# Optimization experiments

Hardware: AMD Instinct MI355X
Metric: run time of the kernel (lower is better)

Reference implementation:

```python
import jax, jax.numpy as jnp
import numpy as np

WINDOW_SIZE = 7
C1 = 0.01 ** 2
C2 = 0.03 ** 2


def _gaussian_window(ws: int) -> jnp.ndarray:
    sigma = ws / 6.0
    coords = jnp.arange(ws, dtype=jnp.float32) - ws // 2
    g = jnp.exp(-coords ** 2 / (2 * sigma ** 2))
    g = g / g.sum()
    k3 = g[:, None, None] * g[None, :, None] * g[None, None, :]
    k3 = k3 / k3.sum()
    return k3.reshape(1, 1, ws, ws, ws)  # OIDHW


def _conv3d_same(x, w):
    pad = WINDOW_SIZE // 2
    return jax.lax.conv_general_dilated(
        x, w, window_strides=(1, 1, 1),
        padding=[(pad, pad)] * 3,
        dimension_numbers=('NCDHW', 'OIDHW', 'NCDHW'))


def setup_inputs() -> dict:
    key = jax.random.key(0)
    k1, k2 = jax.random.split(key)
    shape = (2, 1, 160, 160, 160)
    predicted = jax.random.uniform(k1, shape, dtype=jnp.float32)
    target = jax.random.uniform(k2, shape, dtype=jnp.float32)
    return {"predicted": predicted, "target": target}


def reference(predicted, target):
    window = _gaussian_window(WINDOW_SIZE)
    mu1 = _conv3d_same(predicted, window)
    mu2 = _conv3d_same(target, window)
    mu1_sq = mu1 ** 2
    mu2_sq = mu2 ** 2
    mu1_mu2 = mu1 * mu2
    sigma1_sq = _conv3d_same(predicted ** 2, window) - mu1_sq
    sigma2_sq = _conv3d_same(target ** 2, window) - mu2_sq
    sigma12 = _conv3d_same(predicted * target, window) - mu1_mu2
    ssim_map = ((2 * mu1_mu2 + C1) * (2 * sigma12 + C2)) / (
        (mu1_sq + mu2_sq + C1) * (sigma1_sq + sigma2_sq + C2))
    return 1.0 - ssim_map.mean()
```

## Files before the change

kernel.cpp:

```cpp
#include <hip/hip_runtime.h>
#include <math.h>

#define DD 160
#define HH 160
#define WW 160
#define NB 2
#define NEL (NB*DD*HH*WW)

#define XT 32
#define YT 16
#define ZC 10
#define NTHR 256
#define NZCH (DD/ZC)
#define GX (WW/XT)
#define GY (HH/YT)
#define NBLK (GX*GY*NB*NZCH)
#define NPART NBLK

#define HR 22
#define NJOB (HR*8)
#define CP 35

typedef float v2f __attribute__((ext_vector_type(2)));

struct G7 { float g[7]; };

__global__ __launch_bounds__(NTHR, 4) void ssim_fused(
        const float* __restrict__ p, const float* __restrict__ t,
        float* __restrict__ partial, G7 gw) {
    const int tid = threadIdx.x;
    const int tx  = tid & 31;
    const int tyo = tid >> 5;

    const int flat = blockIdx.x;
    const int w = (flat & 7) * (NBLK / 8) + (flat >> 3);
    const int bx = w % GX;
    const int by = (w / GX) % GY;
    const int bz = w / (GX * GY);

    const int x0 = bx * XT;
    const int y0 = by * YT;
    const int n  = bz / NZCH;
    const int zs = (bz % NZCH) * ZC;

    __shared__ float4 c4[2][HR][CP];

    v2f r01[2][6], r23[2][6];
#pragma unroll
    for (int yo = 0; yo < 2; ++yo)
#pragma unroll
        for (int j = 0; j < 6; ++j) {
            r01[yo][j] = (v2f)(0.f);
            r23[yo][j] = (v2f)(0.f);
        }

    const float C1v = 1e-4f, C2v = 9e-4f;
    float ssum = 0.f;
    const int hw = HH * WW;
    const float* pv = p + (size_t)n * DD * hw;
    const float* tv = t + (size_t)n * DD * hw;

    const int br = tid >> 3;
    const int bxg = tid & 7;
    const int bgy = y0 + br - 3;
    const bool browok = (unsigned)bgy < (unsigned)HH && tid < NJOB;
    const int cbase = x0 + 4 * bxg - 4;
    const int pcr = tx + (tx >> 3);
    bool qok[3];
#pragma unroll
    for (int q = 0; q < 3; ++q)
        qok[q] = browok && (unsigned)(cbase + 4 * q) < (unsigned)WW;

    const float* prow = pv + (size_t)(zs - 3) * hw + bgy * WW;
    const float* trow = tv + (size_t)(zs - 3) * hw + bgy * WW;

    float4 pfa[3], pfb[3];
    auto prefetch = [&](int sx) {
#pragma unroll
        for (int q = 0; q < 3; ++q) {
            pfa[q] = make_float4(0.f, 0.f, 0.f, 0.f);
            pfb[q] = make_float4(0.f, 0.f, 0.f, 0.f);
        }
        if (sx >= 0 && sx < DD && sx < zs + ZC + 3) {
#pragma unroll
            for (int q = 0; q < 3; ++q) {
                if (qok[q]) {
                    pfa[q] = *(const float4*)(prow + cbase + 4 * q);
                    pfb[q] = *(const float4*)(trow + cbase + 4 * q);
                }
            }
        }
    };

    prefetch(zs - 3);

    for (int s = zs - 3; s < zs + ZC + 3; ++s) {
        const int par = s & 1;
        const bool valid = (s >= 0) && (s < DD);

        if (valid) {
            if (tid < NJOB) {
                v2f s01[4], s23[4];
#pragma unroll
                for (int e = 0; e < 4; ++e) { s01[e] = (v2f)(0.f); s23[e] = (v2f)(0.f); }
#pragma unroll
                for (int q = 0; q < 3; ++q) {
                    const float af[4] = {pfa[q].x, pfa[q].y, pfa[q].z, pfa[q].w};
                    const float bf[4] = {pfb[q].x, pfb[q].y, pfb[q].z, pfb[q].w};
#pragma unroll
                    for (int j = 0; j < 4; ++j) {
                        const int i = 4 * q + j;
                        v2f pt; pt[0] = af[j]; pt[1] = bf[j];
                        v2f ud; ud[0] = af[j] + bf[j]; ud[1] = af[j] - bf[j];
                        v2f qu = ud * ud;
#pragma unroll
                        for (int e = 0; e < 4; ++e) {
                            const int k = i - e - 1;
                            if (k >= 0 && k < 7) {
                                s01[e] = gw.g[k] * pt + s01[e];
                                s23[e] = gw.g[k] * qu + s23[e];
                            }
                        }
                    }
                }
#pragma unroll
                for (int e = 0; e < 4; ++e) {
                    int c = 4 * bxg + e;
                    c4[par][br][c + (c >> 3)] =
                        make_float4(s01[e][0], s01[e][1], s23[e][0], s23[e][1]);
                }
            }
            __syncthreads();
        }

        prow += hw; trow += hw;
        prefetch(s + 1);

        v2f m01[2], m23[2];
#pragma unroll
        for (int yo = 0; yo < 2; ++yo) {
            m01[yo] = (v2f)(0.f);
            m23[yo] = (v2f)(0.f);
        }

        if (valid) {
#pragma unroll
            for (int r8 = 0; r8 < 8; ++r8) {
                float4 v = c4[par][2 * tyo + r8][pcr];
                v2f v01; v01[0] = v.x; v01[1] = v.y;
                v2f v23; v23[0] = v.z; v23[1] = v.w;
                if (r8 < 7) {
                    float w2 = gw.g[r8];
                    m01[0] = w2 * v01 + m01[0];
                    m23[0] = w2 * v23 + m23[0];
                }
                if (r8 > 0) {
                    float w2 = gw.g[r8 - 1];
                    m01[1] = w2 * v01 + m01[1];
                    m23[1] = w2 * v23 + m23[1];
                }
            }
        }

#pragma unroll
        for (int yo = 0; yo < 2; ++yo) {
            v2f v01 = m01[yo], v23 = m23[yo];
            v2f cons01 = gw.g[6] * v01 + r01[yo][0];
            v2f cons23 = gw.g[6] * v23 + r23[yo][0];
#pragma unroll
            for (int j = 0; j < 5; ++j) {
                r01[yo][j] = gw.g[5 - j] * v01 + r01[yo][j + 1];
                r23[yo][j] = gw.g[5 - j] * v23 + r23[yo][j + 1];
            }
            r01[yo][5] = gw.g[0] * v01;
            r23[yo][5] = gw.g[0] * v23;

            if (s >= zs + 3) {
                float mu1 = cons01[0], mu2 = cons01[1];
                float Eu  = cons23[0], Ew  = cons23[1];
                float mu12 = mu1 * mu2, mu1sq = mu1 * mu1, mu2sq = mu2 * mu2;
                float sumsq = 0.5f  * (Eu + Ew) - mu1sq - mu2sq;
                float s12   = 0.25f * (Eu - Ew) - mu12;
                float num = (2.f * mu12 + C1v) * (2.f * s12 + C2v);
                float den = (mu1sq + mu2sq + C1v) * (sumsq + C2v);
                ssum += num * __builtin_amdgcn_rcpf(den);
            }
        }
    }

#pragma unroll
    for (int off = 32; off > 0; off >>= 1)
        ssum += __shfl_down(ssum, off, 64);
    __shared__ float wsum[4];
    if ((tid & 63) == 0) wsum[tid >> 6] = ssum;
    __syncthreads();
    if (tid == 0)
        partial[flat] = wsum[0] + wsum[1] + wsum[2] + wsum[3];
}

__global__ __launch_bounds__(256) void ssim_final(
        const float* __restrict__ partial, float* __restrict__ out) {
    float s = 0.f;
    for (int i = threadIdx.x; i < NPART; i += 256) s += partial[i];
#pragma unroll
    for (int off = 32; off > 0; off >>= 1)
        s += __shfl_down(s, off, 64);
    __shared__ float wsum[4];
    int lane = threadIdx.x & 63, wid = threadIdx.x >> 6;
    if (lane == 0) wsum[wid] = s;
    __syncthreads();
    if (threadIdx.x == 0) {
        float tot = wsum[0] + wsum[1] + wsum[2] + wsum[3];
        out[0] = 1.0f - tot / (float)NEL;
    }
}

extern "C" void kernel_launch(void* const* d_in, const int* in_sizes, int n_in,
                              void* d_out, int out_size, void* d_ws, size_t ws_size,
                              hipStream_t stream) {
    const float* p = (const float*)d_in[0];
    const float* t = (const float*)d_in[1];
    float* out = (float*)d_out;
    float* partial = (float*)d_ws;

    G7 gw;
    {
        double s = 0.0, sig = 7.0 / 6.0;
        double g[7];
        for (int i = 0; i < 7; ++i) {
            double d = (double)i - 3.0;
            g[i] = exp(-d * d / (2.0 * sig * sig));
            s += g[i];
        }
        for (int i = 0; i < 7; ++i) gw.g[i] = (float)(g[i] / s);
    }

    ssim_fused<<<NBLK, NTHR, 0, stream>>>(p, t, partial, gw);
    ssim_final<<<1, 256, 0, stream>>>(partial, out);
}
```

Baseline: 144.1 us.

## Software-pipeline the horizontal pass, balance jobs across waves, lengthen z chunks

```diff
diff --git a/kernel.cpp b/kernel.cpp
--- a/kernel.cpp
+++ b/kernel.cpp
@@ -9,7 +9,7 @@
 
 #define XT 32
 #define YT 16
-#define ZC 10
+#define ZC 16
 #define NTHR 256
 #define NZCH (DD/ZC)
 #define GX (WW/XT)
@@ -19,6 +19,7 @@
 
 #define HR 22
 #define NJOB (HR*8)
+#define NJOBW 44
 #define CP 35
 
 typedef float v2f __attribute__((ext_vector_type(2)));
@@ -42,6 +43,7 @@
     const int y0 = by * YT;
     const int n  = bz / NZCH;
     const int zs = (bz % NZCH) * ZC;
+    const int send = zs + ZC + 3;
 
     __shared__ float4 c4[2][HR][CP];
 
@@ -60,10 +62,13 @@
     const float* pv = p + (size_t)n * DD * hw;
     const float* tv = t + (size_t)n * DD * hw;
 
-    const int br = tid >> 3;
-    const int bxg = tid & 7;
+    const int lane = tid & 63, wv = tid >> 6;
+    const int j = wv * NJOBW + lane;
+    const bool jok = lane < NJOBW;
+    const int br  = j >> 3;
+    const int bxg = j & 7;
     const int bgy = y0 + br - 3;
-    const bool browok = (unsigned)bgy < (unsigned)HH && tid < NJOB;
+    const bool browok = jok && (unsigned)bgy < (unsigned)HH;
     const int cbase = x0 + 4 * bxg - 4;
     const int pcr = tx + (tx >> 3);
     bool qok[3];
@@ -81,7 +86,7 @@
             pfa[q] = make_float4(0.f, 0.f, 0.f, 0.f);
             pfb[q] = make_float4(0.f, 0.f, 0.f, 0.f);
         }
-        if (sx >= 0 && sx < DD && sx < zs + ZC + 3) {
+        if (sx >= 0 && sx < DD && sx < send) {
 #pragma unroll
             for (int q = 0; q < 3; ++q) {
                 if (qok[q]) {
@@ -92,49 +97,52 @@
         }
     };
 
-    prefetch(zs - 3);
-
-    for (int s = zs - 3; s < zs + ZC + 3; ++s) {
-        const int par = s & 1;
-        const bool valid = (s >= 0) && (s < DD);
-
-        if (valid) {
-            if (tid < NJOB) {
-                v2f s01[4], s23[4];
-#pragma unroll
-                for (int e = 0; e < 4; ++e) { s01[e] = (v2f)(0.f); s23[e] = (v2f)(0.f); }
-#pragma unroll
-                for (int q = 0; q < 3; ++q) {
-                    const float af[4] = {pfa[q].x, pfa[q].y, pfa[q].z, pfa[q].w};
-                    const float bf[4] = {pfb[q].x, pfb[q].y, pfb[q].z, pfb[q].w};
-#pragma unroll
-                    for (int j = 0; j < 4; ++j) {
-                        const int i = 4 * q + j;
-                        v2f pt; pt[0] = af[j]; pt[1] = bf[j];
-                        v2f ud; ud[0] = af[j] + bf[j]; ud[1] = af[j] - bf[j];
-                        v2f qu = ud * ud;
-#pragma unroll
-                        for (int e = 0; e < 4; ++e) {
-                            const int k = i - e - 1;
-                            if (k >= 0 && k < 7) {
-                                s01[e] = gw.g[k] * pt + s01[e];
-                                s23[e] = gw.g[k] * qu + s23[e];
-                            }
+    auto do_B = [&](int par) {
+        if (jok) {
+            v2f s01[4], s23[4];
+#pragma unroll
+            for (int e = 0; e < 4; ++e) { s01[e] = (v2f)(0.f); s23[e] = (v2f)(0.f); }
+#pragma unroll
+            for (int q = 0; q < 3; ++q) {
+                const float af[4] = {pfa[q].x, pfa[q].y, pfa[q].z, pfa[q].w};
+                const float bf[4] = {pfb[q].x, pfb[q].y, pfb[q].z, pfb[q].w};
+#pragma unroll
+                for (int jj = 0; jj < 4; ++jj) {
+                    const int i = 4 * q + jj;
+                    v2f pt; pt[0] = af[jj]; pt[1] = bf[jj];
+                    v2f ud; ud[0] = af[jj] + bf[jj]; ud[1] = af[jj] - bf[jj];
+                    v2f qu = ud * ud;
+#pragma unroll
+                    for (int e = 0; e < 4; ++e) {
+                        const int k = i - e - 1;
+                        if (k >= 0 && k < 7) {
+                            s01[e] = gw.g[k] * pt + s01[e];
+                            s23[e] = gw.g[k] * qu + s23[e];
                         }
                     }
                 }
-#pragma unroll
-                for (int e = 0; e < 4; ++e) {
-                    int c = 4 * bxg + e;
-                    c4[par][br][c + (c >> 3)] =
-                        make_float4(s01[e][0], s01[e][1], s23[e][0], s23[e][1]);
-                }
-            }
-            __syncthreads();
-        }
+            }
+#pragma unroll
+            for (int e = 0; e < 4; ++e) {
+                int c = 4 * bxg + e;
+                c4[par][br][c + (c >> 3)] =
+                    make_float4(s01[e][0], s01[e][1], s23[e][0], s23[e][1]);
+            }
+        }
+    };
+
+    prefetch(zs - 3);
+    do_B((zs - 3) & 1);
+    prow += hw; trow += hw;
+    prefetch(zs - 2);
+
+    for (int s = zs - 3; s < send; ++s) {
+        __syncthreads();
+
+        if (s + 1 < send) do_B((s + 1) & 1);
 
         prow += hw; trow += hw;
-        prefetch(s + 1);
+        prefetch(s + 2);
 
         v2f m01[2], m23[2];
 #pragma unroll
@@ -142,23 +150,20 @@
             m01[yo] = (v2f)(0.f);
             m23[yo] = (v2f)(0.f);
         }
-
-        if (valid) {
-#pragma unroll
-            for (int r8 = 0; r8 < 8; ++r8) {
-                float4 v = c4[par][2 * tyo + r8][pcr];
-                v2f v01; v01[0] = v.x; v01[1] = v.y;
-                v2f v23; v23[0] = v.z; v23[1] = v.w;
-                if (r8 < 7) {
-                    float w2 = gw.g[r8];
-                    m01[0] = w2 * v01 + m01[0];
-                    m23[0] = w2 * v23 + m23[0];
-                }
-                if (r8 > 0) {
-                    float w2 = gw.g[r8 - 1];
-                    m01[1] = w2 * v01 + m01[1];
-                    m23[1] = w2 * v23 + m23[1];
-                }
+#pragma unroll
+        for (int r8 = 0; r8 < 8; ++r8) {
+            float4 v = c4[s & 1][2 * tyo + r8][pcr];
+            v2f v01; v01[0] = v.x; v01[1] = v.y;
+            v2f v23; v23[0] = v.z; v23[1] = v.w;
+            if (r8 < 7) {
+                float w2 = gw.g[r8];
+                m01[0] = w2 * v01 + m01[0];
+                m23[0] = w2 * v23 + m23[0];
+            }
+            if (r8 > 0) {
+                float w2 = gw.g[r8 - 1];
+                m01[1] = w2 * v01 + m01[1];
+                m23[1] = w2 * v23 + m23[1];
             }
         }
 
@@ -168,9 +173,9 @@
             v2f cons01 = gw.g[6] * v01 + r01[yo][0];
             v2f cons23 = gw.g[6] * v23 + r23[yo][0];
 #pragma unroll
-            for (int j = 0; j < 5; ++j) {
-                r01[yo][j] = gw.g[5 - j] * v01 + r01[yo][j + 1];
-                r23[yo][j] = gw.g[5 - j] * v23 + r23[yo][j + 1];
+            for (int jj = 0; jj < 5; ++jj) {
+                r01[yo][jj] = gw.g[5 - jj] * v01 + r01[yo][jj + 1];
+                r23[yo][jj] = gw.g[5 - jj] * v23 + r23[yo][jj + 1];
             }
             r01[yo][5] = gw.g[0] * v01;
             r23[yo][5] = gw.g[0] * v23;
```

Result: faster. 134.9 us (-6.4%).
